# Kernel optimization log

Hardware: AMD Instinct MI355X
Metric: run time of the kernel (lower is better)

The kernel has to match this reference:

```python
import jax, jax.numpy as jnp
import numpy as np

N = 50000
E = 400000
T = 7
FEAT = 7
H = 64
OUT = 4
LN_EPS = 1e-5


def _w(key, shape, scale=0.1):
    return jax.random.normal(key, shape, jnp.float32) * scale


def setup_inputs() -> dict:
    key = jax.random.key(0)
    ks = list(jax.random.split(key, 16))
    p = {}
    p['x'] = jax.random.normal(ks[0], (N, T, FEAT), jnp.float32)
    p['edge_index'] = jax.random.randint(ks[1], (2, E), 0, N)
    p['edge_weight'] = jax.random.uniform(ks[2], (E,), jnp.float32)
    p['Wg1'] = _w(ks[3], (FEAT, H)); p['bg1'] = jnp.zeros((H,), jnp.float32)
    p['Wg2'] = _w(ks[4], (H, H));    p['bg2'] = jnp.zeros((H,), jnp.float32)
    p['ln_g'] = jnp.ones((H,), jnp.float32); p['ln_b'] = jnp.zeros((H,), jnp.float32)
    p['Wih0'] = _w(ks[5], (4 * H, H)); p['Whh0'] = _w(ks[6], (4 * H, H))
    p['bih0'] = jnp.zeros((4 * H,), jnp.float32); p['bhh0'] = jnp.zeros((4 * H,), jnp.float32)
    p['Wih1'] = _w(ks[7], (4 * H, H)); p['Whh1'] = _w(ks[8], (4 * H, H))
    p['bih1'] = jnp.zeros((4 * H,), jnp.float32); p['bhh1'] = jnp.zeros((4 * H,), jnp.float32)
    p['Wm1'] = _w(ks[9], (H, H // 2));  p['bm1'] = jnp.zeros((H // 2,), jnp.float32)
    p['Wm2'] = _w(ks[10], (H // 2, OUT)); p['bm2'] = jnp.zeros((OUT,), jnp.float32)
    p['Wd1'] = _w(ks[11], (H, H // 4)); p['bd1'] = jnp.zeros((H // 4,), jnp.float32)
    p['Wd2'] = _w(ks[12], (H // 4, OUT)); p['bd2'] = jnp.zeros((OUT,), jnp.float32)
    return p


def gcn_norm(edge_index, edge_weight, n):
    # PyG GCNConv default: add self-loops (weight 1), symmetric normalization
    loop = jnp.arange(n)
    src = jnp.concatenate([edge_index[0], loop])
    dst = jnp.concatenate([edge_index[1], loop])
    w = jnp.concatenate([edge_weight, jnp.ones((n,), edge_weight.dtype)])
    deg = jax.ops.segment_sum(w, dst, num_segments=n)
    dinv = jnp.where(deg > 0, jax.lax.rsqrt(deg), 0.0)
    return src, dst, dinv[src] * w * dinv[dst]


def gcn(h, W, b, src, dst, norm, n):
    h = h @ W                          # [N, H] linear transform first
    m = h[src] * norm[:, None]         # gather + edge scaling  [E', H]
    return jax.ops.segment_sum(m, dst, num_segments=n) + b


def layer_norm(h, g, b):
    mu = jnp.mean(h, -1, keepdims=True)
    v = jnp.mean((h - mu) ** 2, -1, keepdims=True)
    return (h - mu) * jax.lax.rsqrt(v + LN_EPS) * g + b


def lstm_layer(xs, Wih, Whh, bih, bhh):
    # xs: [N, T, H]; torch gate order i, f, g, o
    n = xs.shape[0]
    h0 = jnp.zeros((n, Whh.shape[1]), xs.dtype)
    def step(carry, xt):
        h, c = carry
        gates = xt @ Wih.T + h @ Whh.T + bih + bhh
        i, f, g, o = jnp.split(gates, 4, axis=-1)
        c = jax.nn.sigmoid(f) * c + jax.nn.sigmoid(i) * jnp.tanh(g)
        h = jax.nn.sigmoid(o) * jnp.tanh(c)
        return (h, c), h
    _, hs = jax.lax.scan(step, (h0, h0), jnp.swapaxes(xs, 0, 1))
    return jnp.swapaxes(hs, 0, 1)


def reference(x, edge_index, edge_weight, Wg1, bg1, Wg2, bg2, ln_g, ln_b,
              Wih0, Whh0, bih0, bhh0, Wih1, Whh1, bih1, bhh1,
              Wm1, bm1, Wm2, bm2, Wd1, bd1, Wd2, bd2):
    n = x.shape[0]
    src, dst, norm = gcn_norm(edge_index, edge_weight, n)
    outs = []
    for t in range(x.shape[1]):  # fixed small T=7 (lookback)
        h = gcn(x[:, t, :], Wg1, bg1, src, dst, norm, n)
        h = jax.nn.leaky_relu(h, 0.01)
        # dropout is identity in eval mode
        h = gcn(h, Wg2, bg2, src, dst, norm, n)
        h = jax.nn.leaky_relu(h, 0.01)
        h = layer_norm(h, ln_g, ln_b)
        outs.append(h)
    seq = jnp.stack(outs, axis=1)  # [N, T, H]
    seq = lstm_layer(seq, Wih0, Whh0, bih0, bhh0)
    seq = lstm_layer(seq, Wih1, Whh1, bih1, bhh1)
    f = seq[:, -1, :]
    magnitude = jax.nn.relu(jax.nn.leaky_relu(f @ Wm1 + bm1, 0.01) @ Wm2 + bm2) + 1e-4
    direction = jax.nn.relu(f @ Wd1 + bd1) @ Wd2 + bd2
    return (magnitude, direction)
```

## Files before the change

kernel.cpp:

```cpp
#include <hip/hip_runtime.h>
#include <stdint.h>

#define NN 50000
#define NP 50048
#define EE 400000
#define TT 7
#define LN_EPS 1e-5f

typedef __attribute__((ext_vector_type(8))) short bf16x8;
typedef __attribute__((ext_vector_type(4))) float f32x4;

__device__ __forceinline__ float leaky01(float x){ return x > 0.f ? x : 0.01f*x; }
__device__ __forceinline__ float fastrcp(float x){ return __builtin_amdgcn_rcpf(x); }
__device__ __forceinline__ float sigmoidf(float x){ return fastrcp(1.f+__expf(-x)); }
__device__ __forceinline__ float tanhfast(float x){ return 1.f - 2.f*fastrcp(__expf(2.f*x)+1.f); }
__device__ __forceinline__ unsigned bf16rne(float f){
  unsigned u = __float_as_uint(f);
  return (u + 0x7fffu + ((u>>16)&1u)) >> 16;
}
__device__ __forceinline__ float bfu(unsigned u){ return __uint_as_float(u<<16); }
__device__ __forceinline__ float bfhi(unsigned u){ return __uint_as_float(u & 0xffff0000u); }

__global__ void k_init_deg(float* deg){
  int i = blockIdx.x*blockDim.x + threadIdx.x;
  if (i < NN) deg[i] = 1.0f;
}
__global__ void k_edge_count(const int* __restrict__ src, const int* __restrict__ dst,
                             const float* __restrict__ ew, float* deg, int* counts){
  int e = blockIdx.x*blockDim.x + threadIdx.x;
  if (e < EE){
    int d = dst[e];
    atomicAdd(&deg[d], ew[e]);
    atomicAdd(&counts[d], 1);
  }
}
__global__ __launch_bounds__(256) void k_scan_blk(const int* __restrict__ counts,
                                                  int* locincl, int* bsum, float* deg){
  int tid = threadIdx.x; int i = blockIdx.x*256 + tid;
  if (i < NN) deg[i] = rsqrtf(deg[i]);
  int v = (i < NN) ? counts[i] : 0;
  int lane = tid & 63;
  int val = v;
  #pragma unroll
  for (int off = 1; off < 64; off <<= 1){
    int u = __shfl_up(val, off, 64);
    if (lane >= off) val += u;
  }
  __shared__ int wsum[4];
  if (lane == 63) wsum[tid>>6] = val;
  __syncthreads();
  int w = tid >> 6, pre = 0;
  #pragma unroll
  for (int k = 0; k < 4; ++k) if (k < w) pre += wsum[k];
  int incl = val + pre;
  if (i < NN) locincl[i] = incl;
  if (tid == 255) bsum[blockIdx.x] = incl;
}
__global__ __launch_bounds__(256) void k_scan_top(const int* __restrict__ bsum, int* boff){
  int tid = threadIdx.x;
  int v = (tid < 196) ? bsum[tid] : 0;
  int lane = tid & 63;
  int val = v;
  #pragma unroll
  for (int off = 1; off < 64; off <<= 1){
    int u = __shfl_up(val, off, 64);
    if (lane >= off) val += u;
  }
  __shared__ int wsum[4];
  if (lane == 63) wsum[tid>>6] = val;
  __syncthreads();
  int w = tid >> 6, pre = 0;
  #pragma unroll
  for (int k = 0; k < 4; ++k) if (k < w) pre += wsum[k];
  if (tid < 196) boff[tid] = val + pre - v;
}
__global__ __launch_bounds__(256) void k_scan_fix(const int* __restrict__ locincl,
        const int* __restrict__ boff, const int* __restrict__ counts,
        int* rowptr, int* cursor){
  int i = blockIdx.x*256 + threadIdx.x;
  if (i < NN){
    int r = locincl[i] + boff[blockIdx.x];
    rowptr[i+1] = r;
    cursor[i] = r - counts[i];
  }
  if (i == 0) rowptr[0] = 0;
}
__global__ void k_scatter(const int* __restrict__ src, const int* __restrict__ dst,
                          const float* __restrict__ ew, const float* __restrict__ dinv,
                          int* cursor, int* colsrc, float* enorm){
  int e = blockIdx.x*blockDim.x + threadIdx.x;
  if (e < EE){
    int s = src[e], d = dst[e];
    float nv = dinv[s]*ew[e]*dinv[d];
    int slot = atomicAdd(&cursor[d], 1);
    colsrc[slot] = s;
    enorm[slot] = nv;
  }
}

__global__ void k_prep_wf(const float* __restrict__ Wih0, const float* __restrict__ Whh0,
                          const float* __restrict__ Wih1, const float* __restrict__ Whh1,
                          uint4* WF){
  int idx = blockIdx.x*blockDim.x + threadIdx.x;
  if (idx >= 8192) return;
  int L = idx >> 12;
  int r = idx & 4095;
  int lane = r & 63;
  int e = r >> 6;
  int which = e & 1;
  int cs = e >> 1;
  int s = cs & 1, ct = cs >> 1;
  int row = ct*16 + (lane & 15);
  int kb = s*32 + (lane >> 4)*8;
  const float* W = L ? (which ? Whh1 : Wih1) : (which ? Whh0 : Wih0);
  const float* p = W + row*64 + kb;
  uint4 v;
  v.x = bf16rne(p[0]) | (bf16rne(p[1])<<16);
  v.y = bf16rne(p[2]) | (bf16rne(p[3])<<16);
  v.z = bf16rne(p[4]) | (bf16rne(p[5])<<16);
  v.w = bf16rne(p[6]) | (bf16rne(p[7])<<16);
  WF[idx] = v;
}
__global__ void k_prep_wg2(const float* __restrict__ Wg2, uint4* WG2F){
  int idx = blockIdx.x*blockDim.x + threadIdx.x;
  if (idx >= 512) return;
  int lane = idx & 63, e = idx >> 6;
  int s = e & 1, ct = e >> 1;
  int kb = s*32 + (lane>>4)*8;
  int c = ct*16 + (lane&15);
  uint4 v;
  v.x = bf16rne(Wg2[(kb+0)*64+c]) | (bf16rne(Wg2[(kb+1)*64+c])<<16);
  v.y = bf16rne(Wg2[(kb+2)*64+c]) | (bf16rne(Wg2[(kb+3)*64+c])<<16);
  v.z = bf16rne(Wg2[(kb+4)*64+c]) | (bf16rne(Wg2[(kb+5)*64+c])<<16);
  v.w = bf16rne(Wg2[(kb+6)*64+c]) | (bf16rne(Wg2[(kb+7)*64+c])<<16);
  WG2F[idx] = v;
}
__global__ void k_prep_bias(const float* bih0, const float* bhh0,
                            const float* bih1, const float* bhh1, float* BS){
  int j = threadIdx.x; int L = blockIdx.x;
  if (j < 256) BS[L*256+j] = L ? (bih1[j]+bhh1[j]) : (bih0[j]+bhh0[j]);
}

__global__ __launch_bounds__(256) void k_agg_x(const float* __restrict__ x,
        const float* __restrict__ dinv, const int* __restrict__ rowptr,
        const int* __restrict__ colsrc, const float* __restrict__ enorm,
        float* __restrict__ AX){
  int lane = threadIdx.x & 63, w = threadIdx.x >> 6;
  int i = blockIdx.x*4 + w;
  int beg = rowptr[i], end = rowptr[i+1];
  float di = dinv[i];
  float acc = 0.f;
  if (lane < 49) acc = di*di*x[(size_t)i*49 + lane];
  for (int s = beg; s < end; ++s){
    int cs = colsrc[s]; float wv = enorm[s];
    if (lane < 49) acc += wv * x[(size_t)cs*49 + lane];
  }
  if (lane < 49) AX[(size_t)i*49 + lane] = acc;
}
__global__ __launch_bounds__(256) void k_gcn2_mfma(const float* __restrict__ AX,
        const float* __restrict__ Wg1, const float* __restrict__ bg1,
        const uint4* __restrict__ WG2F, ushort* __restrict__ Z2p){
  __shared__ float sw1[448];
  __shared__ float sb1[64];
  __shared__ float sax[8*56];
  __shared__ __align__(16) ushort srb[64*68];
  int tid = threadIdx.x;
  int lane = tid & 63, w = tid >> 6;
  bf16x8 bw[4][2];
  #pragma unroll
  for (int ct = 0; ct < 4; ++ct)
    #pragma unroll
    for (int s = 0; s < 2; ++s){
      uint4 v = WG2F[(ct*2+s)*64 + lane];
      bw[ct][s] = *(bf16x8*)&v;
    }
  for (int i = tid; i < 448; i += 256) sw1[i] = Wg1[i];
  if (tid < 64) sb1[tid] = bg1[tid];
  int nbase = blockIdx.x*8;
  for (int i = tid; i < 448; i += 256){
    int n = i/56, c = i%56;
    sax[i] = (c < 49) ? AX[(size_t)(nbase+n)*49 + c] : 0.f;
  }
  __syncthreads();
  {
    int node = lane >> 3, t = lane & 7;
    float a[7];
    #pragma unroll
    for (int kk = 0; kk < 7; ++kk) a[kk] = sax[node*56 + t*7 + kk];
    ushort hv[16];
    #pragma unroll
    for (int j = 0; j < 16; ++j){
      int k = w*16 + j;
      float acc = sb1[k];
      #pragma unroll
      for (int kk = 0; kk < 7; ++kk) acc += a[kk]*sw1[kk*64+k];
      hv[j] = (ushort)bf16rne(leaky01(acc));
    }
    uint2* dst = (uint2*)&srb[lane*68 + w*16];
    #pragma unroll
    for (int q = 0; q < 4; ++q){
      uint2 v;
      v.x = (uint)hv[q*4+0] | ((uint)hv[q*4+1]<<16);
      v.y = (uint)hv[q*4+2] | ((uint)hv[q*4+3]<<16);
      dst[q] = v;
    }
  }
  __syncthreads();
  int col = lane & 15, quad = lane >> 4;
  bf16x8 afr[2];
  #pragma unroll
  for (int s = 0; s < 2; ++s){
    const ushort* pr = &srb[(w*16 + col)*68 + s*32 + quad*8];
    uint2 lo = *(const uint2*)pr;
    uint2 hi = *(const uint2*)(pr + 4);
    union { uint u[4]; bf16x8 b; } cv;
    cv.u[0]=lo.x; cv.u[1]=lo.y; cv.u[2]=hi.x; cv.u[3]=hi.y;
    afr[s] = cv.b;
  }
  f32x4 acc[4];
  #pragma unroll
  for (int ct = 0; ct < 4; ++ct) acc[ct] = (f32x4){0.f,0.f,0.f,0.f};
  #pragma unroll
  for (int ct = 0; ct < 4; ++ct)
    #pragma unroll
    for (int s = 0; s < 2; ++s)
      acc[ct] = __builtin_amdgcn_mfma_f32_16x16x32_bf16(afr[s], bw[ct][s], acc[ct], 0,0,0);
  int node = nbase + w*2 + (quad>>1);
  #pragma unroll
  for (int ct = 0; ct < 4; ++ct){
    uint2 v;
    v.x = bf16rne(acc[ct][0]) | (bf16rne(acc[ct][1])<<16);
    v.y = bf16rne(acc[ct][2]) | (bf16rne(acc[ct][3])<<16);
    size_t o = ((size_t)node*64 + ct*16 + col)*8 + (quad&1)*4;
    *(uint2*)(Z2p + o) = v;
  }
}
__global__ __launch_bounds__(256) void k_agg_ln_all(const ushort* __restrict__ Z2p,
        const float* __restrict__ dinv, const int* __restrict__ rowptr,
        const int* __restrict__ colsrc, const float* __restrict__ enorm,
        const float* __restrict__ bg2, const float* __restrict__ lng,
        const float* __restrict__ lnb, ushort* __restrict__ XT){
  int lane = threadIdx.x & 63, w = threadIdx.x >> 6;
  int i = blockIdx.x*4 + w;
  int beg = rowptr[i], end = rowptr[i+1];
  float di = dinv[i];
  float swt = di*di;
  const uint4* zp = (const uint4*)Z2p;
  float acc[7];
  {
    uint4 v = zp[(size_t)i*64 + lane];
    acc[0] = swt*bfu(v.x); acc[1] = swt*bfhi(v.x);
    acc[2] = swt*bfu(v.y); acc[3] = swt*bfhi(v.y);
    acc[4] = swt*bfu(v.z); acc[5] = swt*bfhi(v.z);
    acc[6] = swt*bfu(v.w);
  }
  for (int s = beg; s < end; ++s){
    int cs = colsrc[s]; float wv = enorm[s];
    uint4 v = zp[(size_t)cs*64 + lane];
    acc[0] = fmaf(wv, bfu(v.x),  acc[0]);
    acc[1] = fmaf(wv, bfhi(v.x), acc[1]);
    acc[2] = fmaf(wv, bfu(v.y),  acc[2]);
    acc[3] = fmaf(wv, bfhi(v.y), acc[3]);
    acc[4] = fmaf(wv, bfu(v.z),  acc[4]);
    acc[5] = fmaf(wv, bfhi(v.z), acc[5]);
    acc[6] = fmaf(wv, bfu(v.w),  acc[6]);
  }
  float b2 = bg2[lane], gl = lng[lane], bl = lnb[lane];
  #pragma unroll
  for (int t = 0; t < 7; ++t){
    float a = leaky01(acc[t] + b2);
    float sum = a;
    #pragma unroll
    for (int off = 32; off >= 1; off >>= 1) sum += __shfl_xor(sum, off, 64);
    float mu = sum * (1.f/64.f);
    float d = a - mu;
    float vs = d*d;
    #pragma unroll
    for (int off = 32; off >= 1; off >>= 1) vs += __shfl_xor(vs, off, 64);
    float rs = rsqrtf(vs*(1.f/64.f) + LN_EPS);
    XT[(size_t)t*NP*64 + (size_t)i*64 + lane] = (ushort)bf16rne(d*rs*gl + bl);
  }
}

__global__ __launch_bounds__(256) void k_lstm_seq(const ushort* __restrict__ xin,
        ushort* __restrict__ outbuf, const uint4* __restrict__ WF,
        const float* __restrict__ BS, int mode){
  __shared__ __align__(16) ushort tr[2][32][72];
  int tid = threadIdx.x;
  int lane = tid & 63, cp = tid >> 6;
  int base = blockIdx.x*32;
  int col = lane & 15, quad = lane >> 4;
  bf16x8 bwi[4][2], bwh[4][2];
  #pragma unroll
  for (int g = 0; g < 4; ++g){
    int ct = cp + 4*g;
    #pragma unroll
    for (int s = 0; s < 2; ++s){
      uint4 wi = WF[((ct*2+s)*2+0)*64 + lane];
      uint4 wh = WF[((ct*2+s)*2+1)*64 + lane];
      bwi[g][s] = *(bf16x8*)&wi;
      bwh[g][s] = *(bf16x8*)&wh;
    }
  }
  f32x4 cst[2];
  cst[0] = (f32x4){0.f,0.f,0.f,0.f};
  cst[1] = (f32x4){0.f,0.f,0.f,0.f};
  bf16x8 hfr[2][2];
  #pragma unroll
  for (int mt = 0; mt < 2; ++mt)
    #pragma unroll
    for (int s = 0; s < 2; ++s) hfr[mt][s] = (bf16x8){0,0,0,0,0,0,0,0};
  float bias[4];
  #pragma unroll
  for (int g = 0; g < 4; ++g) bias[g] = BS[(cp + 4*g)*16 + col];

  for (int t = 0; t < 7; ++t){
    int p = t & 1;
    bf16x8 ax[2][2];
    #pragma unroll
    for (int mt = 0; mt < 2; ++mt)
      #pragma unroll
      for (int s = 0; s < 2; ++s)
        ax[mt][s] = *(const bf16x8*)(xin + (size_t)t*NP*64
                        + (size_t)(base + mt*16 + col)*64 + s*32 + quad*8);
    f32x4 acc[2][4];
    #pragma unroll
    for (int g = 0; g < 4; ++g){
      float b = bias[g];
      acc[0][g] = (f32x4){b,b,b,b};
      acc[1][g] = (f32x4){b,b,b,b};
    }
    #pragma unroll
    for (int g = 0; g < 4; ++g){
      #pragma unroll
      for (int s = 0; s < 2; ++s){
        #pragma unroll
        for (int mt = 0; mt < 2; ++mt){
          acc[mt][g] = __builtin_amdgcn_mfma_f32_16x16x32_bf16(ax[mt][s], bwi[g][s], acc[mt][g], 0,0,0);
          acc[mt][g] = __builtin_amdgcn_mfma_f32_16x16x32_bf16(hfr[mt][s], bwh[g][s], acc[mt][g], 0,0,0);
        }
      }
    }
    #pragma unroll
    for (int mt = 0; mt < 2; ++mt){
      #pragma unroll
      for (int r = 0; r < 4; ++r){
        float ig = sigmoidf(acc[mt][0][r]);
        float fg = sigmoidf(acc[mt][1][r]);
        float gg = tanhfast(acc[mt][2][r]);
        float og = sigmoidf(acc[mt][3][r]);
        float cn = fg*cst[mt][r] + ig*gg;
        cst[mt][r] = cn;
        tr[p][mt*16 + quad*4 + r][cp*16 + col] = (ushort)bf16rne(og*tanhfast(cn));
      }
    }
    __syncthreads();
    #pragma unroll
    for (int mt = 0; mt < 2; ++mt)
      #pragma unroll
      for (int s = 0; s < 2; ++s)
        hfr[mt][s] = *(const bf16x8*)&tr[p][mt*16 + col][s*32 + quad*8];
    if (mode == 0 || t == 6){
      int n2 = tid >> 3, off = (tid & 7)*8;
      uint4 v = *(const uint4*)&tr[p][n2][off];
      size_t o = (mode == 0) ? ((size_t)t*NP*64 + (size_t)(base+n2)*64 + off)
                             : ((size_t)(base+n2)*64 + off);
      *(uint4*)(outbuf + o) = v;
    }
  }
}

__global__ __launch_bounds__(256) void k_heads(const ushort* __restrict__ f,
        const float* __restrict__ Wm1, const float* __restrict__ bm1,
        const float* __restrict__ Wm2, const float* __restrict__ bm2,
        const float* __restrict__ Wd1, const float* __restrict__ bd1,
        const float* __restrict__ Wd2, const float* __restrict__ bd2,
        float* __restrict__ out){
  __shared__ float swm1[64*32];
  __shared__ float swm2[32*4];
  __shared__ float swd1[64*16];
  __shared__ float swd2[16*4];
  __shared__ float sbm1[32], sbm2[4], sbd1[16], sbd2[4];
  int tid = threadIdx.x;
  for (int i = tid; i < 2048; i += 256) swm1[i] = Wm1[i];
  for (int i = tid; i < 1024; i += 256) swd1[i] = Wd1[i];
  if (tid < 128) swm2[tid] = Wm2[tid];
  if (tid < 64) swd2[tid] = Wd2[tid];
  if (tid < 32) sbm1[tid] = bm1[tid];
  if (tid < 16) sbd1[tid] = bd1[tid];
  if (tid < 4){ sbm2[tid] = bm2[tid]; sbd2[tid] = bd2[tid]; }
  __syncthreads();
  int n = blockIdx.x*256 + tid;
  if (n >= NN) return;
  float fr[64];
  const uint* f2 = (const uint*)(f + (size_t)n*64);
  #pragma unroll
  for (int i = 0; i < 32; ++i){ uint u = f2[i]; fr[2*i] = bfu(u); fr[2*i+1] = bfhi(u); }
  float m1[32];
  #pragma unroll
  for (int c2 = 0; c2 < 32; ++c2) m1[c2] = sbm1[c2];
  for (int k = 0; k < 64; ++k){
    float fv = fr[k];
    #pragma unroll
    for (int c2 = 0; c2 < 32; ++c2) m1[c2] += fv*swm1[k*32+c2];
  }
  #pragma unroll
  for (int c2 = 0; c2 < 32; ++c2) m1[c2] = leaky01(m1[c2]);
  float mo[4];
  #pragma unroll
  for (int o = 0; o < 4; ++o) mo[o] = sbm2[o];
  for (int c2 = 0; c2 < 32; ++c2){
    float mv = m1[c2];
    #pragma unroll
    for (int o = 0; o < 4; ++o) mo[o] += mv*swm2[c2*4+o];
  }
  float d1[16];
  #pragma unroll
  for (int c2 = 0; c2 < 16; ++c2) d1[c2] = sbd1[c2];
  for (int k = 0; k < 64; ++k){
    float fv = fr[k];
    #pragma unroll
    for (int c2 = 0; c2 < 16; ++c2) d1[c2] += fv*swd1[k*16+c2];
  }
  #pragma unroll
  for (int c2 = 0; c2 < 16; ++c2) d1[c2] = fmaxf(d1[c2], 0.f);
  float dv[4];
  #pragma unroll
  for (int o = 0; o < 4; ++o) dv[o] = sbd2[o];
  for (int c2 = 0; c2 < 16; ++c2){
    float xv = d1[c2];
    #pragma unroll
    for (int o = 0; o < 4; ++o) dv[o] += xv*swd2[c2*4+o];
  }
  float4* o4 = (float4*)out;
  o4[n] = make_float4(fmaxf(mo[0],0.f)+1e-4f, fmaxf(mo[1],0.f)+1e-4f,
                      fmaxf(mo[2],0.f)+1e-4f, fmaxf(mo[3],0.f)+1e-4f);
  o4[NN + n] = make_float4(dv[0], dv[1], dv[2], dv[3]);
}

extern "C" void kernel_launch(void* const* d_in, const int* in_sizes, int n_in,
                              void* d_out, int out_size, void* d_ws, size_t ws_size,
                              hipStream_t stream){
  const float* x    = (const float*)d_in[0];
  const int*   eidx = (const int*)d_in[1];
  const float* ew   = (const float*)d_in[2];
  const float* Wg1  = (const float*)d_in[3];
  const float* bg1  = (const float*)d_in[4];
  const float* Wg2  = (const float*)d_in[5];
  const float* bg2  = (const float*)d_in[6];
  const float* lng  = (const float*)d_in[7];
  const float* lnb  = (const float*)d_in[8];
  const float* Wih0 = (const float*)d_in[9];
  const float* Whh0 = (const float*)d_in[10];
  const float* bih0 = (const float*)d_in[11];
  const float* bhh0 = (const float*)d_in[12];
  const float* Wih1 = (const float*)d_in[13];
  const float* Whh1 = (const float*)d_in[14];
  const float* bih1 = (const float*)d_in[15];
  const float* bhh1 = (const float*)d_in[16];
  const float* Wm1  = (const float*)d_in[17];
  const float* bm1  = (const float*)d_in[18];
  const float* Wm2  = (const float*)d_in[19];
  const float* bm2  = (const float*)d_in[20];
  const float* Wd1  = (const float*)d_in[21];
  const float* bd1  = (const float*)d_in[22];
  const float* Wd2  = (const float*)d_in[23];
  const float* bd2  = (const float*)d_in[24];
  const int* src = eidx;
  const int* dst = eidx + EE;
  float* out = (float*)d_out;

  char* p = (char*)d_ws;
  auto alloc = [&](size_t bytes)->char*{ char* r = p; p += (bytes + 255) & ~(size_t)255; return r; };
  float*  deg     = (float*)alloc((size_t)NN*4);
  float*  enorm   = (float*)alloc((size_t)EE*4);
  int*    counts  = (int*)  alloc((size_t)NN*4);
  int*    rowptr  = (int*)  alloc((size_t)(NN+1)*4);
  int*    cursor  = (int*)  alloc((size_t)NN*4);
  int*    colsrc  = (int*)  alloc((size_t)EE*4);
  int*    locincl = (int*)  alloc((size_t)NN*4);
  int*    bsum    = (int*)  alloc((size_t)256*4);
  int*    boff    = (int*)  alloc((size_t)256*4);
  uint4*  WF      = (uint4*)alloc((size_t)2*4096*16);
  uint4*  WG2F    = (uint4*)alloc((size_t)512*16);
  float*  BS      = (float*)alloc((size_t)2*256*4);
  ushort* h1b     = (ushort*)alloc((size_t)NP*64*2);
  ushort* XT      = (ushort*)alloc((size_t)TT*NP*64*2);
  char*   phase   = alloc((size_t)NN*49*4 + (size_t)NN*64*8*2);
  float*  AX      = (float*)phase;
  ushort* Z2p     = (ushort*)(phase + (size_t)NN*49*4);
  ushort* XT1     = (ushort*)phase;

  hipMemsetAsync(counts, 0, (size_t)NN*4, stream);
  k_init_deg<<<(NN+255)/256, 256, 0, stream>>>(deg);
  k_edge_count<<<(EE+255)/256, 256, 0, stream>>>(src, dst, ew, deg, counts);
  k_scan_blk<<<196, 256, 0, stream>>>(counts, locincl, bsum, deg);
  k_scan_top<<<1, 256, 0, stream>>>(bsum, boff);
  k_scan_fix<<<196, 256, 0, stream>>>(locincl, boff, counts, rowptr, cursor);
  k_scatter<<<(EE+255)/256, 256, 0, stream>>>(src, dst, ew, deg, cursor, colsrc, enorm);
  k_prep_wf<<<32, 256, 0, stream>>>(Wih0, Whh0, Wih1, Whh1, WF);
  k_prep_wg2<<<2, 256, 0, stream>>>(Wg2, WG2F);
  k_prep_bias<<<2, 256, 0, stream>>>(bih0, bhh0, bih1, bhh1, BS);
  k_agg_x<<<NN/4, 256, 0, stream>>>(x, deg, rowptr, colsrc, enorm, AX);

  k_gcn2_mfma<<<NN/8, 256, 0, stream>>>(AX, Wg1, bg1, WG2F, Z2p);
  k_agg_ln_all<<<NN/4, 256, 0, stream>>>(Z2p, deg, rowptr, colsrc, enorm, bg2, lng, lnb, XT);
  k_lstm_seq<<<NP/32, 256, 0, stream>>>(XT,  XT1, WF,        BS,       0);
  k_lstm_seq<<<NP/32, 256, 0, stream>>>(XT1, h1b, WF + 4096, BS + 256, 1);
  k_heads<<<(NN+255)/256, 256, 0, stream>>>(h1b, Wm1, bm1, Wm2, bm2, Wd1, bd1, Wd2, bd2, out);
}
```

Measured before the change: 461.3 us.

## Fuse prep kernels, pack CSR edges, bf16 input copy, fuse both LSTM layers

All small prep kernels and the memset are merged into one launch, which also casts x to bf16 so the first aggregation gathers half the bytes. Column index and edge norm are packed into one uint2 array so each edge is a single load. The two LSTM layers run in one kernel that keeps layer-0 outputs for all 7 steps in shared memory, avoiding the global write and reread of the intermediate sequence. The cost is larger shared memory per block, which may lower occupancy, an extra __syncthreads per step, and bf16 rounding of the raw x input.

```diff
diff --git a/kernel.cpp b/kernel.cpp
--- a/kernel.cpp
+++ b/kernel.cpp
@@ -21,10 +21,59 @@
 __device__ __forceinline__ float bfu(unsigned u){ return __uint_as_float(u<<16); }
 __device__ __forceinline__ float bfhi(unsigned u){ return __uint_as_float(u & 0xffff0000u); }
 
-__global__ void k_init_deg(float* deg){
-  int i = blockIdx.x*blockDim.x + threadIdx.x;
-  if (i < NN) deg[i] = 1.0f;
-}
+__global__ __launch_bounds__(256) void k_prep_all(
+    const float* __restrict__ Wih0, const float* __restrict__ Whh0,
+    const float* __restrict__ Wih1, const float* __restrict__ Whh1,
+    const float* __restrict__ Wg2,
+    const float* __restrict__ bih0, const float* __restrict__ bhh0,
+    const float* __restrict__ bih1, const float* __restrict__ bhh1,
+    const float* __restrict__ x,
+    uint4* __restrict__ WF, uint4* __restrict__ WG2F, float* __restrict__ BS,
+    ushort* __restrict__ xb, float* __restrict__ deg, int* __restrict__ counts){
+  int b = blockIdx.x, tid = threadIdx.x;
+  if (b < 32){
+    int idx = b*256 + tid;
+    int L = idx >> 12;
+    int r = idx & 4095;
+    int lane = r & 63;
+    int e = r >> 6;
+    int which = e & 1;
+    int cs = e >> 1;
+    int s = cs & 1, ct = cs >> 1;
+    int row = ct*16 + (lane & 15);
+    int kb = s*32 + (lane >> 4)*8;
+    const float* W = L ? (which ? Whh1 : Wih1) : (which ? Whh0 : Wih0);
+    const float* p = W + row*64 + kb;
+    uint4 v;
+    v.x = bf16rne(p[0]) | (bf16rne(p[1])<<16);
+    v.y = bf16rne(p[2]) | (bf16rne(p[3])<<16);
+    v.z = bf16rne(p[4]) | (bf16rne(p[5])<<16);
+    v.w = bf16rne(p[6]) | (bf16rne(p[7])<<16);
+    WF[idx] = v;
+  } else if (b < 34){
+    int idx = (b-32)*256 + tid;
+    int lane = idx & 63, e = idx >> 6;
+    int s = e & 1, ct = e >> 1;
+    int kb = s*32 + (lane>>4)*8;
+    int c = ct*16 + (lane&15);
+    uint4 v;
+    v.x = bf16rne(Wg2[(kb+0)*64+c]) | (bf16rne(Wg2[(kb+1)*64+c])<<16);
+    v.y = bf16rne(Wg2[(kb+2)*64+c]) | (bf16rne(Wg2[(kb+3)*64+c])<<16);
+    v.z = bf16rne(Wg2[(kb+4)*64+c]) | (bf16rne(Wg2[(kb+5)*64+c])<<16);
+    v.w = bf16rne(Wg2[(kb+6)*64+c]) | (bf16rne(Wg2[(kb+7)*64+c])<<16);
+    WG2F[idx] = v;
+  } else if (b < 36){
+    int L = b - 34;
+    BS[L*256+tid] = L ? (bih1[tid]+bhh1[tid]) : (bih0[tid]+bhh0[tid]);
+  } else if (b < 232){
+    int i = (b-36)*256 + tid;
+    if (i < NN){ deg[i] = 1.0f; counts[i] = 0; }
+  } else {
+    int i = (b-232)*256 + tid;
+    if (i < NN*49) xb[i] = (ushort)bf16rne(x[i]);
+  }
+}
+
 __global__ void k_edge_count(const int* __restrict__ src, const int* __restrict__ dst,
                              const float* __restrict__ ew, float* deg, int* counts){
   int e = blockIdx.x*blockDim.x + threadIdx.x;
@@ -87,73 +136,29 @@
 }
 __global__ void k_scatter(const int* __restrict__ src, const int* __restrict__ dst,
                           const float* __restrict__ ew, const float* __restrict__ dinv,
-                          int* cursor, int* colsrc, float* enorm){
+                          int* cursor, uint2* e2){
   int e = blockIdx.x*blockDim.x + threadIdx.x;
   if (e < EE){
     int s = src[e], d = dst[e];
     float nv = dinv[s]*ew[e]*dinv[d];
     int slot = atomicAdd(&cursor[d], 1);
-    colsrc[slot] = s;
-    enorm[slot] = nv;
-  }
-}
-
-__global__ void k_prep_wf(const float* __restrict__ Wih0, const float* __restrict__ Whh0,
-                          const float* __restrict__ Wih1, const float* __restrict__ Whh1,
-                          uint4* WF){
-  int idx = blockIdx.x*blockDim.x + threadIdx.x;
-  if (idx >= 8192) return;
-  int L = idx >> 12;
-  int r = idx & 4095;
-  int lane = r & 63;
-  int e = r >> 6;
-  int which = e & 1;
-  int cs = e >> 1;
-  int s = cs & 1, ct = cs >> 1;
-  int row = ct*16 + (lane & 15);
-  int kb = s*32 + (lane >> 4)*8;
-  const float* W = L ? (which ? Whh1 : Wih1) : (which ? Whh0 : Wih0);
-  const float* p = W + row*64 + kb;
-  uint4 v;
-  v.x = bf16rne(p[0]) | (bf16rne(p[1])<<16);
-  v.y = bf16rne(p[2]) | (bf16rne(p[3])<<16);
-  v.z = bf16rne(p[4]) | (bf16rne(p[5])<<16);
-  v.w = bf16rne(p[6]) | (bf16rne(p[7])<<16);
-  WF[idx] = v;
-}
-__global__ void k_prep_wg2(const float* __restrict__ Wg2, uint4* WG2F){
-  int idx = blockIdx.x*blockDim.x + threadIdx.x;
-  if (idx >= 512) return;
-  int lane = idx & 63, e = idx >> 6;
-  int s = e & 1, ct = e >> 1;
-  int kb = s*32 + (lane>>4)*8;
-  int c = ct*16 + (lane&15);
-  uint4 v;
-  v.x = bf16rne(Wg2[(kb+0)*64+c]) | (bf16rne(Wg2[(kb+1)*64+c])<<16);
-  v.y = bf16rne(Wg2[(kb+2)*64+c]) | (bf16rne(Wg2[(kb+3)*64+c])<<16);
-  v.z = bf16rne(Wg2[(kb+4)*64+c]) | (bf16rne(Wg2[(kb+5)*64+c])<<16);
-  v.w = bf16rne(Wg2[(kb+6)*64+c]) | (bf16rne(Wg2[(kb+7)*64+c])<<16);
-  WG2F[idx] = v;
-}
-__global__ void k_prep_bias(const float* bih0, const float* bhh0,
-                            const float* bih1, const float* bhh1, float* BS){
-  int j = threadIdx.x; int L = blockIdx.x;
-  if (j < 256) BS[L*256+j] = L ? (bih1[j]+bhh1[j]) : (bih0[j]+bhh0[j]);
-}
-
-__global__ __launch_bounds__(256) void k_agg_x(const float* __restrict__ x,
+    e2[slot] = make_uint2((uint)s, __float_as_uint(nv));
+  }
+}
+
+__global__ __launch_bounds__(256) void k_agg_x(const ushort* __restrict__ xb,
         const float* __restrict__ dinv, const int* __restrict__ rowptr,
-        const int* __restrict__ colsrc, const float* __restrict__ enorm,
-        float* __restrict__ AX){
+        const uint2* __restrict__ e2, float* __restrict__ AX){
   int lane = threadIdx.x & 63, w = threadIdx.x >> 6;
   int i = blockIdx.x*4 + w;
   int beg = rowptr[i], end = rowptr[i+1];
   float di = dinv[i];
   float acc = 0.f;
-  if (lane < 49) acc = di*di*x[(size_t)i*49 + lane];
+  if (lane < 49) acc = di*di*bfu(xb[(size_t)i*49 + lane]);
   for (int s = beg; s < end; ++s){
-    int cs = colsrc[s]; float wv = enorm[s];
-    if (lane < 49) acc += wv * x[(size_t)cs*49 + lane];
+    uint2 e = e2[s];
+    int cs = (int)e.x; float wv = __uint_as_float(e.y);
+    if (lane < 49) acc += wv * bfu(xb[(size_t)cs*49 + lane]);
   }
   if (lane < 49) AX[(size_t)i*49 + lane] = acc;
 }
@@ -237,7 +242,7 @@
 }
 __global__ __launch_bounds__(256) void k_agg_ln_all(const ushort* __restrict__ Z2p,
         const float* __restrict__ dinv, const int* __restrict__ rowptr,
-        const int* __restrict__ colsrc, const float* __restrict__ enorm,
+        const uint2* __restrict__ e2,
         const float* __restrict__ bg2, const float* __restrict__ lng,
         const float* __restrict__ lnb, ushort* __restrict__ XT){
   int lane = threadIdx.x & 63, w = threadIdx.x >> 6;
@@ -255,7 +260,8 @@
     acc[6] = swt*bfu(v.w);
   }
   for (int s = beg; s < end; ++s){
-    int cs = colsrc[s]; float wv = enorm[s];
+    uint2 e = e2[s];
+    int cs = (int)e.x; float wv = __uint_as_float(e.y);
     uint4 v = zp[(size_t)cs*64 + lane];
     acc[0] = fmaf(wv, bfu(v.x),  acc[0]);
     acc[1] = fmaf(wv, bfhi(v.x), acc[1]);
@@ -282,92 +288,99 @@
   }
 }
 
-__global__ __launch_bounds__(256) void k_lstm_seq(const ushort* __restrict__ xin,
-        ushort* __restrict__ outbuf, const uint4* __restrict__ WF,
-        const float* __restrict__ BS, int mode){
-  __shared__ __align__(16) ushort tr[2][32][72];
+__global__ __launch_bounds__(256) void k_lstm_both(const ushort* __restrict__ xin,
+        ushort* __restrict__ h1out, const uint4* __restrict__ WF,
+        const float* __restrict__ BS){
+  __shared__ __align__(16) ushort XL[7][32][72];
   int tid = threadIdx.x;
   int lane = tid & 63, cp = tid >> 6;
   int base = blockIdx.x*32;
   int col = lane & 15, quad = lane >> 4;
-  bf16x8 bwi[4][2], bwh[4][2];
-  #pragma unroll
-  for (int g = 0; g < 4; ++g){
-    int ct = cp + 4*g;
-    #pragma unroll
-    for (int s = 0; s < 2; ++s){
-      uint4 wi = WF[((ct*2+s)*2+0)*64 + lane];
-      uint4 wh = WF[((ct*2+s)*2+1)*64 + lane];
-      bwi[g][s] = *(bf16x8*)&wi;
-      bwh[g][s] = *(bf16x8*)&wh;
+  for (int L = 0; L < 2; ++L){
+    bf16x8 bwi[4][2], bwh[4][2];
+    const uint4* wf = WF + L*4096;
+    #pragma unroll
+    for (int g = 0; g < 4; ++g){
+      int ct = cp + 4*g;
+      #pragma unroll
+      for (int s = 0; s < 2; ++s){
+        uint4 wi = wf[((ct*2+s)*2+0)*64 + lane];
+        uint4 wh = wf[((ct*2+s)*2+1)*64 + lane];
+        bwi[g][s] = *(bf16x8*)&wi;
+        bwh[g][s] = *(bf16x8*)&wh;
+      }
     }
-  }
-  f32x4 cst[2];
-  cst[0] = (f32x4){0.f,0.f,0.f,0.f};
-  cst[1] = (f32x4){0.f,0.f,0.f,0.f};
-  bf16x8 hfr[2][2];
-  #pragma unroll
-  for (int mt = 0; mt < 2; ++mt)
-    #pragma unroll
-    for (int s = 0; s < 2; ++s) hfr[mt][s] = (bf16x8){0,0,0,0,0,0,0,0};
-  float bias[4];
-  #pragma unroll
-  for (int g = 0; g < 4; ++g) bias[g] = BS[(cp + 4*g)*16 + col];
-
-  for (int t = 0; t < 7; ++t){
-    int p = t & 1;
-    bf16x8 ax[2][2];
+    float bias[4];
+    #pragma unroll
+    for (int g = 0; g < 4; ++g) bias[g] = BS[L*256 + (cp + 4*g)*16 + col];
+    f32x4 cst[2];
+    cst[0] = (f32x4){0.f,0.f,0.f,0.f};
+    cst[1] = (f32x4){0.f,0.f,0.f,0.f};
+    bf16x8 hfr[2][2];
     #pragma unroll
     for (int mt = 0; mt < 2; ++mt)
       #pragma unroll
-      for (int s = 0; s < 2; ++s)
-        ax[mt][s] = *(const bf16x8*)(xin + (size_t)t*NP*64
-                        + (size_t)(base + mt*16 + col)*64 + s*32 + quad*8);
-    f32x4 acc[2][4];
-    #pragma unroll
-    for (int g = 0; g < 4; ++g){
-      float b = bias[g];
-      acc[0][g] = (f32x4){b,b,b,b};
-      acc[1][g] = (f32x4){b,b,b,b};
-    }
-    #pragma unroll
-    for (int g = 0; g < 4; ++g){
-      #pragma unroll
-      for (int s = 0; s < 2; ++s){
+      for (int s = 0; s < 2; ++s) hfr[mt][s] = (bf16x8){0,0,0,0,0,0,0,0};
+
+    for (int t = 0; t < 7; ++t){
+      bf16x8 ax[2][2];
+      if (L == 0){
         #pragma unroll
-        for (int mt = 0; mt < 2; ++mt){
-          acc[mt][g] = __builtin_amdgcn_mfma_f32_16x16x32_bf16(ax[mt][s], bwi[g][s], acc[mt][g], 0,0,0);
-          acc[mt][g] = __builtin_amdgcn_mfma_f32_16x16x32_bf16(hfr[mt][s], bwh[g][s], acc[mt][g], 0,0,0);
+        for (int mt = 0; mt < 2; ++mt)
+          #pragma unroll
+          for (int s = 0; s < 2; ++s)
+            ax[mt][s] = *(const bf16x8*)(xin + (size_t)t*NP*64
+                            + (size_t)(base + mt*16 + col)*64 + s*32 + quad*8);
+      } else {
+        #pragma unroll
+        for (int mt = 0; mt < 2; ++mt)
+          #pragma unroll
+          for (int s = 0; s < 2; ++s)
+            ax[mt][s] = *(const bf16x8*)&XL[t][mt*16 + col][s*32 + quad*8];
+      }
+      f32x4 acc[2][4];
+      #pragma unroll
+      for (int g = 0; g < 4; ++g){
+        float b = bias[g];
+        acc[0][g] = (f32x4){b,b,b,b};
+        acc[1][g] = (f32x4){b,b,b,b};
+      }
+      #pragma unroll
+      for (int g = 0; g < 4; ++g){
+        #pragma unroll
+        for (int s = 0; s < 2; ++s){
+          #pragma unroll
+          for (int mt = 0; mt < 2; ++mt){
+            acc[mt][g] = __builtin_amdgcn_mfma_f32_16x16x32_bf16(ax[mt][s], bwi[g][s], acc[mt][g], 0,0,0);
+            acc[mt][g] = __builtin_amdgcn_mfma_f32_16x16x32_bf16(hfr[mt][s], bwh[g][s], acc[mt][g], 0,0,0);
+          }
         }
       }
+      __syncthreads();
+      #pragma unroll
+      for (int mt = 0; mt < 2; ++mt){
+        #pragma unroll
+        for (int r = 0; r < 4; ++r){
+          float ig = sigmoidf(acc[mt][0][r]);
+          float fg = sigmoidf(acc[mt][1][r]);
+          float gg = tanhfast(acc[mt][2][r]);
+          float og = sigmoidf(acc[mt][3][r]);
+          float cn = fg*cst[mt][r] + ig*gg;
+          cst[mt][r] = cn;
+          XL[t][mt*16 + quad*4 + r][cp*16 + col] = (ushort)bf16rne(og*tanhfast(cn));
+        }
+      }
+      __syncthreads();
+      #pragma unroll
+      for (int mt = 0; mt < 2; ++mt)
+        #pragma unroll
+        for (int s = 0; s < 2; ++s)
+          hfr[mt][s] = *(const bf16x8*)&XL[t][mt*16 + col][s*32 + quad*8];
     }
-    #pragma unroll
-    for (int mt = 0; mt < 2; ++mt){
-      #pragma unroll
-      for (int r = 0; r < 4; ++r){
-        float ig = sigmoidf(acc[mt][0][r]);
-        float fg = sigmoidf(acc[mt][1][r]);
-        float gg = tanhfast(acc[mt][2][r]);
-        float og = sigmoidf(acc[mt][3][r]);
-        float cn = fg*cst[mt][r] + ig*gg;
-        cst[mt][r] = cn;
-        tr[p][mt*16 + quad*4 + r][cp*16 + col] = (ushort)bf16rne(og*tanhfast(cn));
-      }
-    }
-    __syncthreads();
-    #pragma unroll
-    for (int mt = 0; mt < 2; ++mt)
-      #pragma unroll
-      for (int s = 0; s < 2; ++s)
-        hfr[mt][s] = *(const bf16x8*)&tr[p][mt*16 + col][s*32 + quad*8];
-    if (mode == 0 || t == 6){
-      int n2 = tid >> 3, off = (tid & 7)*8;
-      uint4 v = *(const uint4*)&tr[p][n2][off];
-      size_t o = (mode == 0) ? ((size_t)t*NP*64 + (size_t)(base+n2)*64 + off)
-                             : ((size_t)(base+n2)*64 + off);
-      *(uint4*)(outbuf + o) = v;
-    }
-  }
+  }
+  int n2 = tid >> 3, off = (tid & 7)*8;
+  uint4 v = *(const uint4*)&XL[6][n2][off];
+  *(uint4*)(h1out + (size_t)(base+n2)*64 + off) = v;
 }
 
 __global__ __launch_bounds__(256) void k_heads(const ushort* __restrict__ f,
@@ -473,39 +486,33 @@
   char* p = (char*)d_ws;
   auto alloc = [&](size_t bytes)->char*{ char* r = p; p += (bytes + 255) & ~(size_t)255; return r; };
   float*  deg     = (float*)alloc((size_t)NN*4);
-  float*  enorm   = (float*)alloc((size_t)EE*4);
   int*    counts  = (int*)  alloc((size_t)NN*4);
   int*    rowptr  = (int*)  alloc((size_t)(NN+1)*4);
   int*    cursor  = (int*)  alloc((size_t)NN*4);
-  int*    colsrc  = (int*)  alloc((size_t)EE*4);
   int*    locincl = (int*)  alloc((size_t)NN*4);
   int*    bsum    = (int*)  alloc((size_t)256*4);
   int*    boff    = (int*)  alloc((size_t)256*4);
+  uint2*  e2      = (uint2*)alloc((size_t)EE*8);
   uint4*  WF      = (uint4*)alloc((size_t)2*4096*16);
   uint4*  WG2F    = (uint4*)alloc((size_t)512*16);
   float*  BS      = (float*)alloc((size_t)2*256*4);
+  ushort* xb      = (ushort*)alloc((size_t)NN*49*2);
   ushort* h1b     = (ushort*)alloc((size_t)NP*64*2);
   ushort* XT      = (ushort*)alloc((size_t)TT*NP*64*2);
-  char*   phase   = alloc((size_t)NN*49*4 + (size_t)NN*64*8*2);
-  float*  AX      = (float*)phase;
-  ushort* Z2p     = (ushort*)(phase + (size_t)NN*49*4);
-  ushort* XT1     = (ushort*)phase;
-
-  hipMemsetAsync(counts, 0, (size_t)NN*4, stream);
-  k_init_deg<<<(NN+255)/256, 256, 0, stream>>>(deg);
+  float*  AX      = (float*)alloc((size_t)NN*49*4);
+  ushort* Z2p     = (ushort*)alloc((size_t)NN*64*8*2);
+
+  int xblocks = (NN*49 + 255)/256;
+  k_prep_all<<<232 + xblocks, 256, 0, stream>>>(Wih0, Whh0, Wih1, Whh1, Wg2,
+      bih0, bhh0, bih1, bhh1, x, WF, WG2F, BS, xb, deg, counts);
   k_edge_count<<<(EE+255)/256, 256, 0, stream>>>(src, dst, ew, deg, counts);
   k_scan_blk<<<196, 256, 0, stream>>>(counts, locincl, bsum, deg);
   k_scan_top<<<1, 256, 0, stream>>>(bsum, boff);
   k_scan_fix<<<196, 256, 0, stream>>>(locincl, boff, counts, rowptr, cursor);
-  k_scatter<<<(EE+255)/256, 256, 0, stream>>>(src, dst, ew, deg, cursor, colsrc, enorm);
-  k_prep_wf<<<32, 256, 0, stream>>>(Wih0, Whh0, Wih1, Whh1, WF);
-  k_prep_wg2<<<2, 256, 0, stream>>>(Wg2, WG2F);
-  k_prep_bias<<<2, 256, 0, stream>>>(bih0, bhh0, bih1, bhh1, BS);
-  k_agg_x<<<NN/4, 256, 0, stream>>>(x, deg, rowptr, colsrc, enorm, AX);
-
+  k_scatter<<<(EE+255)/256, 256, 0, stream>>>(src, dst, ew, deg, cursor, e2);
+  k_agg_x<<<NN/4, 256, 0, stream>>>(xb, deg, rowptr, e2, AX);
   k_gcn2_mfma<<<NN/8, 256, 0, stream>>>(AX, Wg1, bg1, WG2F, Z2p);
-  k_agg_ln_all<<<NN/4, 256, 0, stream>>>(Z2p, deg, rowptr, colsrc, enorm, bg2, lng, lnb, XT);
-  k_lstm_seq<<<NP/32, 256, 0, stream>>>(XT,  XT1, WF,        BS,       0);
-  k_lstm_seq<<<NP/32, 256, 0, stream>>>(XT1, h1b, WF + 4096, BS + 256, 1);
+  k_agg_ln_all<<<NN/4, 256, 0, stream>>>(Z2p, deg, rowptr, e2, bg2, lng, lnb, XT);
+  k_lstm_both<<<NP/32, 256, 0, stream>>>(XT, h1b, WF, BS);
   k_heads<<<(NN+255)/256, 256, 0, stream>>>(h1b, Wm1, bm1, Wm2, bm2, Wd1, bd1, Wd2, bd2, out);
 }
```

Result: faster. 428.9 us (-7.0%).
